# Performance work log

Measured on AMD Instinct MI355X. Metric: run time of the kernel, lower is better.

The kernel has to match this reference:

```python
import jax, jax.numpy as jnp
import numpy as np

EMBED_DIM = 768
NUM_HEADS = 12
HEAD_DIM = EMBED_DIM // NUM_HEADS
ROPE_BASE = 10000.0


def setup_inputs() -> dict:
    key = jax.random.key(0)
    k1, k2, k3, k4, k5 = jax.random.split(key, 5)
    B, S, E = 1, 4096, EMBED_DIM
    x = jax.random.normal(k1, (B, S, E), dtype=jnp.float32)
    # causal mask: 1 where attend allowed, 0 elsewhere
    mask = jnp.tril(jnp.ones((S, S), dtype=jnp.int32))
    scale = 1.0 / np.sqrt(E)
    Wqkv = jax.random.normal(k2, (E, 3 * E), dtype=jnp.float32) * scale
    bqkv = jax.random.normal(k3, (3 * E,), dtype=jnp.float32) * 0.01
    Wout = jax.random.normal(k4, (E, E), dtype=jnp.float32) * scale
    bout = jax.random.normal(k5, (E,), dtype=jnp.float32) * 0.01
    return {"x": x, "mask": mask, "Wqkv": Wqkv, "bqkv": bqkv, "Wout": Wout, "bout": bout}


def _rope_cos_sin(seq_len, dtype):
    inv_freq = 1.0 / (ROPE_BASE ** (jnp.arange(0, HEAD_DIM, 2, dtype=jnp.float32) / HEAD_DIM))
    t = jnp.arange(seq_len, dtype=dtype)
    freqs = jnp.outer(t, inv_freq.astype(dtype))  # [S, Dh/2]
    emb = jnp.concatenate([freqs, freqs], axis=-1)  # [S, Dh]
    return jnp.cos(emb), jnp.sin(emb)


def _rotate_half(u):
    u1, u2 = jnp.split(u, 2, axis=-1)
    return jnp.concatenate([-u2, u1], axis=-1)


def reference(x, mask, Wqkv, bqkv, Wout, bout):
    B, S, E = x.shape
    H, Dh = NUM_HEADS, HEAD_DIM
    qkv = x @ Wqkv + bqkv  # [B, S, 3E]
    qkv = qkv.reshape(B, S, 3, H, Dh).transpose(2, 0, 3, 1, 4)  # [3, B, H, S, Dh]
    Q, K, V = qkv[0], qkv[1], qkv[2]
    # RoPE
    cos, sin = _rope_cos_sin(S, x.dtype)  # [S, Dh]
    cos = cos[None, None]
    sin = sin[None, None]
    Q = Q * cos + _rotate_half(Q) * sin
    K = K * cos + _rotate_half(K) * sin
    scores = jnp.einsum('bhsd,bhtd->bhst', Q, K) / jnp.sqrt(jnp.asarray(Dh, x.dtype))
    scores = jnp.where(mask[None, None] == 0, jnp.finfo(x.dtype).min, scores)
    attn = jax.nn.softmax(scores, axis=-1)  # dropout p=0 (eval) -> identity
    out = jnp.einsum('bhst,bhtd->bhsd', attn, V)  # [B, H, S, Dh]
    out = out.transpose(0, 2, 1, 3).reshape(B, S, E)
    return out @ Wout + bout
```

## Files before the change

### kernel.cpp

```cpp
#include <hip/hip_runtime.h>

typedef unsigned short u16;
typedef unsigned int   u32;
using short8 = __attribute__((ext_vector_type(8))) short;
using f32x4  = __attribute__((ext_vector_type(4))) float;
using f32x16 = __attribute__((ext_vector_type(16))) float;
using u32x4  = __attribute__((ext_vector_type(4))) unsigned int;

#define S_LEN 4096
#define EMB   768
#define NH    12
#define DH    64

#define QSCALE 0.18033688011112042f

__device__ __forceinline__ u16 f2bf(float f) {
  unsigned int u = __builtin_bit_cast(unsigned int, f);
  u += 0x7fffu + ((u >> 16) & 1u);
  return (u16)(u >> 16);
}

__device__ __forceinline__ u32 cvtpk(float lo, float hi) {
  u32 r;
  asm("v_cvt_pk_bf16_f32 %0, %1, %2" : "=v"(r) : "v"(lo), "v"(hi));
  return r;
}

__device__ __forceinline__ float fexp2(float x) {
#if __has_builtin(__builtin_amdgcn_exp2f)
  return __builtin_amdgcn_exp2f(x);
#else
  return exp2f(x);
#endif
}

__device__ __forceinline__ f32x4 mfma16(short8 a, short8 b, f32x4 c) {
  return __builtin_amdgcn_mfma_f32_16x16x32_bf16(a, b, c, 0, 0, 0);
}
__device__ __forceinline__ f32x16 mfma32(short8 a, short8 b, f32x16 c) {
  return __builtin_amdgcn_mfma_f32_32x32x16_bf16(a, b, c, 0, 0, 0);
}


__global__ void k_conv_x(const float* __restrict__ x, u16* __restrict__ xb, int n) {
  int i = blockIdx.x * 256 + threadIdx.x;
  if (i < n) xb[i] = f2bf(x[i]);
}

__global__ __launch_bounds__(256) void k_transpose_w(const float* __restrict__ w,
                                                     u16* __restrict__ wt,
                                                     int rows, int cols) {
  __shared__ float tile[32][33];
  int tx = threadIdx.x & 31, ty = threadIdx.x >> 5;
  int kb = blockIdx.x * 32;
  int nb = blockIdx.y * 32;
#pragma unroll
  for (int j = 0; j < 4; j++)
    tile[ty + 8 * j][tx] = w[(size_t)(kb + ty + 8 * j) * cols + nb + tx];
  __syncthreads();
#pragma unroll
  for (int j = 0; j < 4; j++)
    wt[(size_t)(nb + ty + 8 * j) * rows + kb + tx] = f2bf(tile[tx][ty + 8 * j]);
}

__global__ __launch_bounds__(256) void k_qkv(const u16* __restrict__ A,
                                             const u16* __restrict__ Bt,
                                             const float* __restrict__ bias,
                                             u16* __restrict__ Qb,
                                             u16* __restrict__ Kb,
                                             u16* __restrict__ Vt) {
  __shared__ u16 As[128][40];
  __shared__ u16 Bs[128][40];
  int t = threadIdx.x;
  int w = t >> 6, lane = t & 63, g = lane >> 4, c = lane & 15;
  int wr = w >> 1, wc = w & 1;
  int bm = blockIdx.x * 128, bn = blockIdx.y * 128;

  f32x4 acc[4][4];
#pragma unroll
  for (int m = 0; m < 4; m++)
#pragma unroll
    for (int n = 0; n < 4; n++) acc[m][n] = (f32x4){0.f, 0.f, 0.f, 0.f};

  int srow = t >> 1, sseg = (t & 1) * 16;
  for (int bk = 0; bk < EMB; bk += 32) {
    const u16* ga = A  + (size_t)(bm + srow) * EMB + bk + sseg;
    const u16* gb = Bt + (size_t)(bn + srow) * EMB + bk + sseg;
    short8 a0 = *(const short8*)ga, a1 = *(const short8*)(ga + 8);
    short8 b0 = *(const short8*)gb, b1 = *(const short8*)(gb + 8);
    __syncthreads();
    *(short8*)&As[srow][sseg] = a0; *(short8*)&As[srow][sseg + 8] = a1;
    *(short8*)&Bs[srow][sseg] = b0; *(short8*)&Bs[srow][sseg + 8] = b1;
    __syncthreads();
    short8 af[4], bf[4];
#pragma unroll
    for (int m = 0; m < 4; m++) af[m] = *(const short8*)&As[wr * 64 + m * 16 + c][g * 8];
#pragma unroll
    for (int n = 0; n < 4; n++) bf[n] = *(const short8*)&Bs[wc * 64 + n * 16 + c][g * 8];
#pragma unroll
    for (int m = 0; m < 4; m++)
#pragma unroll
      for (int n = 0; n < 4; n++) acc[m][n] = mfma16(af[m], bf[n], acc[m][n]);
  }

  int colbase = bn + wc * 64;
  int sec = colbase / EMB;
  int hh  = (colbase % EMB) / DH;
  float qs = (sec == 0) ? QSCALE : 1.0f;
  float invf[2];
#pragma unroll
  for (int n = 0; n < 2; n++) {
    int d1 = n * 16 + c;
    invf[n] = exp2f(-(float)d1 * (13.287712379549449f / 32.0f));
  }
#pragma unroll
  for (int m = 0; m < 4; m++) {
    int rowb = bm + wr * 64 + m * 16 + 4 * g;
#pragma unroll
    for (int e = 0; e < 4; e++) {
      int srw = rowb + e;
      float v[4];
#pragma unroll
      for (int n = 0; n < 4; n++) v[n] = acc[m][n][e] + bias[colbase + n * 16 + c];
      if (sec == 2) {
#pragma unroll
        for (int n = 0; n < 4; n++)
          Vt[(size_t)(hh * DH + n * 16 + c) * S_LEN + srw] = f2bf(v[n]);
      } else {
        u16* dst = (sec == 0) ? Qb : Kb;
        size_t base = ((size_t)hh * S_LEN + srw) * DH;
#pragma unroll
        for (int n = 0; n < 2; n++) {
          int d1 = n * 16 + c;
          float ang = (float)srw * invf[n];
          float sn, cs;
          sincosf(ang, &sn, &cs);
          float o1 = (v[n] * cs - v[n + 2] * sn) * qs;
          float o2 = (v[n + 2] * cs + v[n] * sn) * qs;
          dst[base + d1]      = f2bf(o1);
          dst[base + d1 + 32] = f2bf(o2);
        }
      }
    }
  }
}


template<bool MASKED>
__device__ __forceinline__ void attn_tile(int kv0, int qi, int half,
    const u16* __restrict__ Kh, const u16* __restrict__ Vh,
    short8 qf0, short8 qf1, short8 qf2, short8 qf3,
    f32x16& acc0, f32x16& acc1, float& m, float& l) {
  const u16* kp = Kh + (size_t)(kv0 + qi) * DH + half * 8;
  short8 k0 = *(const short8*)(kp);
  short8 k1 = *(const short8*)(kp + 16);
  short8 k2 = *(const short8*)(kp + 32);
  short8 k3 = *(const short8*)(kp + 48);
  f32x16 sc = {0,0,0,0,0,0,0,0,0,0,0,0,0,0,0,0};
  sc = mfma32(k0, qf0, sc);
  sc = mfma32(k1, qf1, sc);
  sc = mfma32(k2, qf2, sc);
  sc = mfma32(k3, qf3, sc);
  if (MASKED) {
#pragma unroll
    for (int i = 0; i < 16; i++) {
      int kl = (i & 3) + 8 * (i >> 2) + 4 * half;
      if (kl > qi) sc[i] = -1e30f;
    }
  }
  float t0 = fmaxf(fmaxf(sc[0], sc[1]), fmaxf(sc[2], sc[3]));
  float t1 = fmaxf(fmaxf(sc[4], sc[5]), fmaxf(sc[6], sc[7]));
  float t2 = fmaxf(fmaxf(sc[8], sc[9]), fmaxf(sc[10], sc[11]));
  float t3 = fmaxf(fmaxf(sc[12], sc[13]), fmaxf(sc[14], sc[15]));
  float pmax = fmaxf(fmaxf(t0, t1), fmaxf(t2, t3));
  float rmax = fmaxf(pmax, __shfl_xor(pmax, 32));
  if (__any(rmax > m + 8.0f)) {
    float mn = fmaxf(m, rmax);
    float f = fexp2(m - mn);
    m = mn; l *= f;
#pragma unroll
    for (int i = 0; i < 16; i++) { acc0[i] *= f; acc1[i] *= f; }
  }
  f32x16 p;
#pragma unroll
  for (int i = 0; i < 16; i++) p[i] = fexp2(sc[i] - m);
  l += ((p[0] + p[1]) + (p[2] + p[3])) + ((p[4] + p[5]) + (p[6] + p[7]))
     + ((p[8] + p[9]) + (p[10] + p[11])) + ((p[12] + p[13]) + (p[14] + p[15]));
  u32 w0 = cvtpk(p[0], p[1]),  w1 = cvtpk(p[2], p[3]);
  u32 w2 = cvtpk(p[4], p[5]),  w3 = cvtpk(p[6], p[7]);
  u32 w4 = cvtpk(p[8], p[9]),  w5 = cvtpk(p[10], p[11]);
  u32 w6 = cvtpk(p[12], p[13]), w7 = cvtpk(p[14], p[15]);
  u32 x0 = (u32)__shfl_xor((int)w0, 32), x1 = (u32)__shfl_xor((int)w1, 32);
  u32 x2 = (u32)__shfl_xor((int)w2, 32), x3 = (u32)__shfl_xor((int)w3, 32);
  u32 x4 = (u32)__shfl_xor((int)w4, 32), x5 = (u32)__shfl_xor((int)w5, 32);
  u32 x6 = (u32)__shfl_xor((int)w6, 32), x7 = (u32)__shfl_xor((int)w7, 32);
  bool hi = (half != 0);
  u32x4 f0 = { hi ? x2 : w0, hi ? x3 : w1, hi ? w2 : x0, hi ? w3 : x1 };
  u32x4 f1 = { hi ? x6 : w4, hi ? x7 : w5, hi ? w6 : x4, hi ? w7 : x5 };
  short8 pa0 = __builtin_bit_cast(short8, f0);
  short8 pa1 = __builtin_bit_cast(short8, f1);
  const u16* vp = Vh + (size_t)qi * S_LEN + kv0 + half * 8;
  short8 v00 = *(const short8*)(vp);
  short8 v01 = *(const short8*)(vp + 16);
  short8 v10 = *(const short8*)(vp + (size_t)32 * S_LEN);
  short8 v11 = *(const short8*)(vp + (size_t)32 * S_LEN + 16);
  acc0 = mfma32(v00, pa0, acc0);
  acc0 = mfma32(v01, pa1, acc0);
  acc1 = mfma32(v10, pa0, acc1);
  acc1 = mfma32(v11, pa1, acc1);
}

__global__ __launch_bounds__(256, 4) void k_attn(const u16* __restrict__ Q,
                                                 const u16* __restrict__ K,
                                                 const u16* __restrict__ Vt,
                                                 u16* __restrict__ O) {
  __shared__ float Lacc[3][64][33];
  __shared__ float Lml[2][3][32];

  int t = threadIdx.x;
  int w = t >> 6, lane = t & 63;
  int qi = lane & 31, half = lane >> 5;
  int b = blockIdx.x;
  int h = b % NH;
  int qb = 127 - b / NH;

  const u16* Qh = Q  + (size_t)h * S_LEN * DH;
  const u16* Kh = K  + (size_t)h * S_LEN * DH;
  const u16* Vh = Vt + (size_t)h * DH * S_LEN;

  const u16* qp = Qh + (size_t)(qb * 32 + qi) * DH + half * 8;
  short8 qf0 = *(const short8*)(qp);
  short8 qf1 = *(const short8*)(qp + 16);
  short8 qf2 = *(const short8*)(qp + 32);
  short8 qf3 = *(const short8*)(qp + 48);

  f32x16 acc0 = {0,0,0,0,0,0,0,0,0,0,0,0,0,0,0,0};
  f32x16 acc1 = {0,0,0,0,0,0,0,0,0,0,0,0,0,0,0,0};
  float m = -1e30f, l = 0.f;

  int nt = qb + 1;
  int ck = (nt + 3) >> 2;
  int start = w * ck;
  int end   = min(start + ck, nt);
  int endu  = min(end, nt - 1);
  for (int tt = start; tt < endu; tt++)
    attn_tile<false>(tt * 32, qi, half, Kh, Vh, qf0, qf1, qf2, qf3, acc0, acc1, m, l);
  if (start < nt && end == nt)
    attn_tile<true>((nt - 1) * 32, qi, half, Kh, Vh, qf0, qf1, qf2, qf3, acc0, acc1, m, l);

  float l2 = l + __shfl_xor(l, 32);
  if (w > 0) {
#pragma unroll
    for (int i = 0; i < 16; i++) {
      Lacc[w - 1][lane][i]      = acc0[i];
      Lacc[w - 1][lane][16 + i] = acc1[i];
    }
    if (half == 0) { Lml[0][w - 1][qi] = m; Lml[1][w - 1][qi] = l2; }
  }
  __syncthreads();
  if (w == 0) {
    float mw[3], lw[3];
    float M = m;
#pragma unroll
    for (int j = 0; j < 3; j++) { mw[j] = Lml[0][j][qi]; lw[j] = Lml[1][j][qi]; M = fmaxf(M, mw[j]); }
    float f0 = fexp2(m - M);
    float ltot = l2 * f0;
#pragma unroll
    for (int i = 0; i < 16; i++) { acc0[i] *= f0; acc1[i] *= f0; }
#pragma unroll
    for (int j = 0; j < 3; j++) {
      float fj = fexp2(mw[j] - M);
      ltot += lw[j] * fj;
#pragma unroll
      for (int i = 0; i < 16; i++) {
        acc0[i] += fj * Lacc[j][lane][i];
        acc1[i] += fj * Lacc[j][lane][16 + i];
      }
    }
    float rl = 1.0f / ltot;
    u16* orow = O + (size_t)(qb * 32 + qi) * EMB + h * DH;
#pragma unroll
    for (int i = 0; i < 16; i += 2) {
      int dl = (i & 3) + 8 * (i >> 2) + 4 * half;
      u32 wa = cvtpk(acc0[i] * rl, acc0[i + 1] * rl);
      u32 wb = cvtpk(acc1[i] * rl, acc1[i + 1] * rl);
      *(u32*)(orow + dl)      = wa;
      *(u32*)(orow + 32 + dl) = wb;
    }
  }
}

__global__ __launch_bounds__(256) void k_out(const u16* __restrict__ A,
                                             const u16* __restrict__ Bt,
                                             const float* __restrict__ bias,
                                             float* __restrict__ out) {
  __shared__ u16 As[128][40];
  __shared__ u16 Bs[128][40];
  int t = threadIdx.x;
  int w = t >> 6, lane = t & 63, g = lane >> 4, c = lane & 15;
  int wr = w >> 1, wc = w & 1;
  int bm = blockIdx.x * 128, bn = blockIdx.y * 128;

  f32x4 acc[4][4];
#pragma unroll
  for (int m = 0; m < 4; m++)
#pragma unroll
    for (int n = 0; n < 4; n++) acc[m][n] = (f32x4){0.f, 0.f, 0.f, 0.f};

  int srow = t >> 1, sseg = (t & 1) * 16;
  for (int bk = 0; bk < EMB; bk += 32) {
    const u16* ga = A  + (size_t)(bm + srow) * EMB + bk + sseg;
    const u16* gb = Bt + (size_t)(bn + srow) * EMB + bk + sseg;
    short8 a0 = *(const short8*)ga, a1 = *(const short8*)(ga + 8);
    short8 b0 = *(const short8*)gb, b1 = *(const short8*)(gb + 8);
    __syncthreads();
    *(short8*)&As[srow][sseg] = a0; *(short8*)&As[srow][sseg + 8] = a1;
    *(short8*)&Bs[srow][sseg] = b0; *(short8*)&Bs[srow][sseg + 8] = b1;
    __syncthreads();
    short8 af[4], bf[4];
#pragma unroll
    for (int m = 0; m < 4; m++) af[m] = *(const short8*)&As[wr * 64 + m * 16 + c][g * 8];
#pragma unroll
    for (int n = 0; n < 4; n++) bf[n] = *(const short8*)&Bs[wc * 64 + n * 16 + c][g * 8];
#pragma unroll
    for (int m = 0; m < 4; m++)
#pragma unroll
      for (int n = 0; n < 4; n++) acc[m][n] = mfma16(af[m], bf[n], acc[m][n]);
  }
  int colbase = bn + wc * 64;
#pragma unroll
  for (int m = 0; m < 4; m++) {
    int rowb = bm + wr * 64 + m * 16 + 4 * g;
#pragma unroll
    for (int e = 0; e < 4; e++) {
      int srw = rowb + e;
#pragma unroll
      for (int n = 0; n < 4; n++) {
        int col = colbase + n * 16 + c;
        out[(size_t)srw * EMB + col] = acc[m][n][e] + bias[col];
      }
    }
  }
}


extern "C" void kernel_launch(void* const* d_in, const int* in_sizes, int n_in,
                              void* d_out, int out_size, void* d_ws, size_t ws_size,
                              hipStream_t stream) {
  const float* x    = (const float*)d_in[0];
  const float* Wqkv = (const float*)d_in[2];
  const float* bqkv = (const float*)d_in[3];
  const float* Wout = (const float*)d_in[4];
  const float* bout = (const float*)d_in[5];
  float* out = (float*)d_out;

  char* ws = (char*)d_ws;
  u16* xb     = (u16*)(ws);
  u16* wqkvt  = (u16*)(ws + 6291456);
  u16* woutt  = (u16*)(ws + 9830400);
  u16* Qb     = (u16*)(ws + 11010048);
  u16* Kb     = (u16*)(ws + 17301504);
  u16* Vtb    = (u16*)(ws + 23592960);
  u16* Ob     = (u16*)(ws + 29884416);

  k_conv_x<<<(S_LEN * EMB + 255) / 256, 256, 0, stream>>>(x, xb, S_LEN * EMB);
  k_transpose_w<<<dim3(EMB / 32, 3 * EMB / 32), 256, 0, stream>>>(Wqkv, wqkvt, EMB, 3 * EMB);
  k_transpose_w<<<dim3(EMB / 32, EMB / 32), 256, 0, stream>>>(Wout, woutt, EMB, EMB);

  k_qkv<<<dim3(32, 18), 256, 0, stream>>>(xb, wqkvt, bqkv, Qb, Kb, Vtb);
  k_attn<<<NH * 128, 256, 0, stream>>>(Qb, Kb, Vtb, Ob);
  k_out<<<dim3(32, 6), 256, 0, stream>>>(Ob, woutt, bout, out);
}
```

Measured before the change: 180.6 us.

## Process two KV tiles per attention iteration with MFMA priority hints

Adds a two-tile attention step that loads K and V for 64 keys at once, interleaves the independent score MFMAs, and does one running-max update per pair of tiles. It also hoists the V loads ahead of the softmax math and wraps MFMA groups in s_setprio to favour matrix issue. The aim is more memory-level parallelism and fewer max/rescale rounds per key. In exchange, register pressure rises, so launch bounds drop from 4 to 3 waves' worth of blocks, which may cut occupancy.

Result: no change. 178.2 us (-1.3%).

```diff
diff --git a/kernel.cpp b/kernel.cpp
--- a/kernel.cpp
+++ b/kernel.cpp
@@ -26,6 +26,13 @@
   return r;
 }
 
+__device__ __forceinline__ float pr_max(float v) {
+  return fmaxf(v, __shfl_xor(v, 32));
+}
+__device__ __forceinline__ float pr_add(float v) {
+  return v + __shfl_xor(v, 32);
+}
+
 __device__ __forceinline__ float fexp2(float x) {
 #if __has_builtin(__builtin_amdgcn_exp2f)
   return __builtin_amdgcn_exp2f(x);
@@ -39,6 +46,13 @@
 }
 __device__ __forceinline__ f32x16 mfma32(short8 a, short8 b, f32x16 c) {
   return __builtin_amdgcn_mfma_f32_32x32x16_bf16(a, b, c, 0, 0, 0);
+}
+
+__device__ __forceinline__ short8 pack_frag(u32 w0, u32 w1, u32 w2, u32 w3, bool hi) {
+  u32 x0 = (u32)__shfl_xor((int)w0, 32), x1 = (u32)__shfl_xor((int)w1, 32);
+  u32 x2 = (u32)__shfl_xor((int)w2, 32), x3 = (u32)__shfl_xor((int)w3, 32);
+  u32x4 f = { hi ? x2 : w0, hi ? x3 : w1, hi ? w2 : x0, hi ? w3 : x1 };
+  return __builtin_bit_cast(short8, f);
 }
 
 
@@ -156,61 +170,140 @@
   short8 k1 = *(const short8*)(kp + 16);
   short8 k2 = *(const short8*)(kp + 32);
   short8 k3 = *(const short8*)(kp + 48);
+  __builtin_amdgcn_s_setprio(1);
   f32x16 sc = {0,0,0,0,0,0,0,0,0,0,0,0,0,0,0,0};
   sc = mfma32(k0, qf0, sc);
   sc = mfma32(k1, qf1, sc);
   sc = mfma32(k2, qf2, sc);
   sc = mfma32(k3, qf3, sc);
-  if (MASKED) {
-#pragma unroll
-    for (int i = 0; i < 16; i++) {
-      int kl = (i & 3) + 8 * (i >> 2) + 4 * half;
-      if (kl > qi) sc[i] = -1e30f;
-    }
-  }
-  float t0 = fmaxf(fmaxf(sc[0], sc[1]), fmaxf(sc[2], sc[3]));
-  float t1 = fmaxf(fmaxf(sc[4], sc[5]), fmaxf(sc[6], sc[7]));
-  float t2 = fmaxf(fmaxf(sc[8], sc[9]), fmaxf(sc[10], sc[11]));
-  float t3 = fmaxf(fmaxf(sc[12], sc[13]), fmaxf(sc[14], sc[15]));
-  float pmax = fmaxf(fmaxf(t0, t1), fmaxf(t2, t3));
-  float rmax = fmaxf(pmax, __shfl_xor(pmax, 32));
-  if (__any(rmax > m + 8.0f)) {
-    float mn = fmaxf(m, rmax);
-    float f = fexp2(m - mn);
-    m = mn; l *= f;
-#pragma unroll
-    for (int i = 0; i < 16; i++) { acc0[i] *= f; acc1[i] *= f; }
-  }
-  f32x16 p;
-#pragma unroll
-  for (int i = 0; i < 16; i++) p[i] = fexp2(sc[i] - m);
-  l += ((p[0] + p[1]) + (p[2] + p[3])) + ((p[4] + p[5]) + (p[6] + p[7]))
-     + ((p[8] + p[9]) + (p[10] + p[11])) + ((p[12] + p[13]) + (p[14] + p[15]));
-  u32 w0 = cvtpk(p[0], p[1]),  w1 = cvtpk(p[2], p[3]);
-  u32 w2 = cvtpk(p[4], p[5]),  w3 = cvtpk(p[6], p[7]);
-  u32 w4 = cvtpk(p[8], p[9]),  w5 = cvtpk(p[10], p[11]);
-  u32 w6 = cvtpk(p[12], p[13]), w7 = cvtpk(p[14], p[15]);
-  u32 x0 = (u32)__shfl_xor((int)w0, 32), x1 = (u32)__shfl_xor((int)w1, 32);
-  u32 x2 = (u32)__shfl_xor((int)w2, 32), x3 = (u32)__shfl_xor((int)w3, 32);
-  u32 x4 = (u32)__shfl_xor((int)w4, 32), x5 = (u32)__shfl_xor((int)w5, 32);
-  u32 x6 = (u32)__shfl_xor((int)w6, 32), x7 = (u32)__shfl_xor((int)w7, 32);
-  bool hi = (half != 0);
-  u32x4 f0 = { hi ? x2 : w0, hi ? x3 : w1, hi ? w2 : x0, hi ? w3 : x1 };
-  u32x4 f1 = { hi ? x6 : w4, hi ? x7 : w5, hi ? w6 : x4, hi ? w7 : x5 };
-  short8 pa0 = __builtin_bit_cast(short8, f0);
-  short8 pa1 = __builtin_bit_cast(short8, f1);
+  __builtin_amdgcn_s_setprio(0);
   const u16* vp = Vh + (size_t)qi * S_LEN + kv0 + half * 8;
   short8 v00 = *(const short8*)(vp);
   short8 v01 = *(const short8*)(vp + 16);
   short8 v10 = *(const short8*)(vp + (size_t)32 * S_LEN);
   short8 v11 = *(const short8*)(vp + (size_t)32 * S_LEN + 16);
+  if (MASKED) {
+#pragma unroll
+    for (int i = 0; i < 16; i++) {
+      int kl = (i & 3) + 8 * (i >> 2) + 4 * half;
+      if (kl > qi) sc[i] = -1e30f;
+    }
+  }
+  float t0 = fmaxf(fmaxf(sc[0], sc[1]), fmaxf(sc[2], sc[3]));
+  float t1 = fmaxf(fmaxf(sc[4], sc[5]), fmaxf(sc[6], sc[7]));
+  float t2 = fmaxf(fmaxf(sc[8], sc[9]), fmaxf(sc[10], sc[11]));
+  float t3 = fmaxf(fmaxf(sc[12], sc[13]), fmaxf(sc[14], sc[15]));
+  float rmax = pr_max(fmaxf(fmaxf(t0, t1), fmaxf(t2, t3)));
+  if (__any(rmax > m + 8.0f)) {
+    float mn = fmaxf(m, rmax);
+    float f = fexp2(m - mn);
+    m = mn; l *= f;
+#pragma unroll
+    for (int i = 0; i < 16; i++) { acc0[i] *= f; acc1[i] *= f; }
+  }
+  f32x16 p;
+#pragma unroll
+  for (int i = 0; i < 16; i++) p[i] = fexp2(sc[i] - m);
+  l += ((p[0] + p[1]) + (p[2] + p[3])) + ((p[4] + p[5]) + (p[6] + p[7]))
+     + ((p[8] + p[9]) + (p[10] + p[11])) + ((p[12] + p[13]) + (p[14] + p[15]));
+  bool hi = (half != 0);
+  short8 pa0 = pack_frag(cvtpk(p[0], p[1]),   cvtpk(p[2], p[3]),
+                         cvtpk(p[4], p[5]),   cvtpk(p[6], p[7]), hi);
+  short8 pa1 = pack_frag(cvtpk(p[8], p[9]),   cvtpk(p[10], p[11]),
+                         cvtpk(p[12], p[13]), cvtpk(p[14], p[15]), hi);
+  __builtin_amdgcn_s_setprio(1);
   acc0 = mfma32(v00, pa0, acc0);
   acc0 = mfma32(v01, pa1, acc0);
   acc1 = mfma32(v10, pa0, acc1);
   acc1 = mfma32(v11, pa1, acc1);
-}
-
-__global__ __launch_bounds__(256, 4) void k_attn(const u16* __restrict__ Q,
+  __builtin_amdgcn_s_setprio(0);
+}
+
+__device__ __forceinline__ void attn_tile2(int kv0, int qi, int half,
+    const u16* __restrict__ Kh, const u16* __restrict__ Vh,
+    short8 qf0, short8 qf1, short8 qf2, short8 qf3,
+    f32x16& acc0, f32x16& acc1, float& m, float& l) {
+  const u16* kpa = Kh + (size_t)(kv0 + qi) * DH + half * 8;
+  const u16* kpb = kpa + (size_t)32 * DH;
+  short8 ka0 = *(const short8*)(kpa);
+  short8 ka1 = *(const short8*)(kpa + 16);
+  short8 ka2 = *(const short8*)(kpa + 32);
+  short8 ka3 = *(const short8*)(kpa + 48);
+  short8 kb0 = *(const short8*)(kpb);
+  short8 kb1 = *(const short8*)(kpb + 16);
+  short8 kb2 = *(const short8*)(kpb + 32);
+  short8 kb3 = *(const short8*)(kpb + 48);
+  __builtin_amdgcn_s_setprio(1);
+  f32x16 sa = {0,0,0,0,0,0,0,0,0,0,0,0,0,0,0,0};
+  f32x16 sb = {0,0,0,0,0,0,0,0,0,0,0,0,0,0,0,0};
+  sa = mfma32(ka0, qf0, sa);
+  sb = mfma32(kb0, qf0, sb);
+  sa = mfma32(ka1, qf1, sa);
+  sb = mfma32(kb1, qf1, sb);
+  sa = mfma32(ka2, qf2, sa);
+  sb = mfma32(kb2, qf2, sb);
+  sa = mfma32(ka3, qf3, sa);
+  sb = mfma32(kb3, qf3, sb);
+  __builtin_amdgcn_s_setprio(0);
+  const u16* vpa = Vh + (size_t)qi * S_LEN + kv0 + half * 8;
+  const u16* vpb = vpa + 32;
+  short8 va00 = *(const short8*)(vpa);
+  short8 va01 = *(const short8*)(vpa + 16);
+  short8 va10 = *(const short8*)(vpa + (size_t)32 * S_LEN);
+  short8 va11 = *(const short8*)(vpa + (size_t)32 * S_LEN + 16);
+  short8 vb00 = *(const short8*)(vpb);
+  short8 vb01 = *(const short8*)(vpb + 16);
+  short8 vb10 = *(const short8*)(vpb + (size_t)32 * S_LEN);
+  short8 vb11 = *(const short8*)(vpb + (size_t)32 * S_LEN + 16);
+  float t0 = fmaxf(fmaxf(sa[0], sa[1]), fmaxf(sa[2], sa[3]));
+  float t1 = fmaxf(fmaxf(sa[4], sa[5]), fmaxf(sa[6], sa[7]));
+  float t2 = fmaxf(fmaxf(sa[8], sa[9]), fmaxf(sa[10], sa[11]));
+  float t3 = fmaxf(fmaxf(sa[12], sa[13]), fmaxf(sa[14], sa[15]));
+  float u0 = fmaxf(fmaxf(sb[0], sb[1]), fmaxf(sb[2], sb[3]));
+  float u1 = fmaxf(fmaxf(sb[4], sb[5]), fmaxf(sb[6], sb[7]));
+  float u2 = fmaxf(fmaxf(sb[8], sb[9]), fmaxf(sb[10], sb[11]));
+  float u3 = fmaxf(fmaxf(sb[12], sb[13]), fmaxf(sb[14], sb[15]));
+  float rmax = pr_max(fmaxf(fmaxf(fmaxf(t0, t1), fmaxf(t2, t3)),
+                            fmaxf(fmaxf(u0, u1), fmaxf(u2, u3))));
+  if (__any(rmax > m + 8.0f)) {
+    float mn = fmaxf(m, rmax);
+    float f = fexp2(m - mn);
+    m = mn; l *= f;
+#pragma unroll
+    for (int i = 0; i < 16; i++) { acc0[i] *= f; acc1[i] *= f; }
+  }
+  f32x16 pa, pb;
+#pragma unroll
+  for (int i = 0; i < 16; i++) pa[i] = fexp2(sa[i] - m);
+#pragma unroll
+  for (int i = 0; i < 16; i++) pb[i] = fexp2(sb[i] - m);
+  float la = ((pa[0] + pa[1]) + (pa[2] + pa[3])) + ((pa[4] + pa[5]) + (pa[6] + pa[7]))
+           + ((pa[8] + pa[9]) + (pa[10] + pa[11])) + ((pa[12] + pa[13]) + (pa[14] + pa[15]));
+  float lb = ((pb[0] + pb[1]) + (pb[2] + pb[3])) + ((pb[4] + pb[5]) + (pb[6] + pb[7]))
+           + ((pb[8] + pb[9]) + (pb[10] + pb[11])) + ((pb[12] + pb[13]) + (pb[14] + pb[15]));
+  l += la + lb;
+  bool hi = (half != 0);
+  short8 fa0 = pack_frag(cvtpk(pa[0], pa[1]),   cvtpk(pa[2], pa[3]),
+                         cvtpk(pa[4], pa[5]),   cvtpk(pa[6], pa[7]), hi);
+  short8 fa1 = pack_frag(cvtpk(pa[8], pa[9]),   cvtpk(pa[10], pa[11]),
+                         cvtpk(pa[12], pa[13]), cvtpk(pa[14], pa[15]), hi);
+  short8 fb0 = pack_frag(cvtpk(pb[0], pb[1]),   cvtpk(pb[2], pb[3]),
+                         cvtpk(pb[4], pb[5]),   cvtpk(pb[6], pb[7]), hi);
+  short8 fb1 = pack_frag(cvtpk(pb[8], pb[9]),   cvtpk(pb[10], pb[11]),
+                         cvtpk(pb[12], pb[13]), cvtpk(pb[14], pb[15]), hi);
+  __builtin_amdgcn_s_setprio(1);
+  acc0 = mfma32(va00, fa0, acc0);
+  acc1 = mfma32(va10, fa0, acc1);
+  acc0 = mfma32(va01, fa1, acc0);
+  acc1 = mfma32(va11, fa1, acc1);
+  acc0 = mfma32(vb00, fb0, acc0);
+  acc1 = mfma32(vb10, fb0, acc1);
+  acc0 = mfma32(vb01, fb1, acc0);
+  acc1 = mfma32(vb11, fb1, acc1);
+  __builtin_amdgcn_s_setprio(0);
+}
+
+__global__ __launch_bounds__(256, 3) void k_attn(const u16* __restrict__ Q,
                                                  const u16* __restrict__ K,
                                                  const u16* __restrict__ Vt,
                                                  u16* __restrict__ O) {
@@ -243,12 +336,16 @@
   int start = w * ck;
   int end   = min(start + ck, nt);
   int endu  = min(end, nt - 1);
-  for (int tt = start; tt < endu; tt++)
+  int tt = start;
+#pragma unroll 1
+  for (; tt + 1 < endu; tt += 2)
+    attn_tile2(tt * 32, qi, half, Kh, Vh, qf0, qf1, qf2, qf3, acc0, acc1, m, l);
+  for (; tt < endu; tt++)
     attn_tile<false>(tt * 32, qi, half, Kh, Vh, qf0, qf1, qf2, qf3, acc0, acc1, m, l);
   if (start < nt && end == nt)
     attn_tile<true>((nt - 1) * 32, qi, half, Kh, Vh, qf0, qf1, qf2, qf3, acc0, acc1, m, l);
 
-  float l2 = l + __shfl_xor(l, 32);
+  float l2 = pr_add(l);
   if (w > 0) {
 #pragma unroll
     for (int i = 0; i < 16; i++) {
```
